# Performance work log

Hardware: AMD Instinct MI355X
Metric: run time of the kernel (lower is better)

The kernel has to match this reference:

```python
import jax, jax.numpy as jnp
import numpy as np
from jax.scipy.linalg import expm

M = 8          # number of mixture models
S = 4          # alphabet size (nucleotides)
N_LEAVES = 20  # taxa
K = 19         # internal nodes (caterpillar binary tree)
BATCH = 200000 # alignment sites


def _build_tree():
    # Caterpillar rooted binary tree: internal node n has children (leaf0, leaf1);
    # internal node n+j has children (internal n+j-1, leaf j+1). T[b, a] = branch length b->a.
    n, k = N_LEAVES, K
    N = n + k
    rng = np.random.default_rng(0)
    T = np.zeros((N, N), dtype=np.float32)
    T[0, n] = rng.uniform(0.05, 1.0)
    T[1, n] = rng.uniform(0.05, 1.0)
    for j in range(1, k):
        a = n + j
        T[a - 1, a] = rng.uniform(0.05, 1.0)
        T[j + 1, a] = rng.uniform(0.05, 1.0)
    return T


def setup_inputs() -> dict:
    key = jax.random.key(0)
    k1, k2 = jax.random.split(key, 2)
    X = jax.random.uniform(k1, (BATCH, N_LEAVES, S), dtype=jnp.float32)
    rates = jax.random.uniform(k2, (M, S * (S - 1) // 2), dtype=jnp.float32)
    pi_inv = jnp.full((M, S - 1), 1.0 / (np.sqrt(S) - 1.0), dtype=jnp.float32)
    rho = jnp.ones((M,), dtype=jnp.float32)
    T = _build_tree()  # numpy: tree structure is static config, not a traced tensor
    return {"X": X, "rates": rates, "pi_inv": pi_inv, "rho": rho, "T": T}


def _inv_stereographic_projection(y):
    ns = jnp.sum(y ** 2, axis=-1)
    return jnp.concatenate([2.0 * y, (ns - 1.0)[..., None]], axis=-1) / (ns + 1.0)[..., None]


def _rate_matrices(rates_sq, pi):
    # rates_sq: [M, s(s-1)/2], pi: [M, s] -> Q: [M, s, s]
    iu, ju = np.triu_indices(S, 1)
    Q = jnp.zeros((M, S, S), rates_sq.dtype).at[:, iu, ju].set(rates_sq)
    Q = Q + jnp.swapaxes(Q, 1, 2)                    # symmetrize
    Q = Q * pi[:, None, :]                           # stationary probabilities
    new_diag = -jnp.sum(Q, axis=2)                   # row sums -> diagonal
    ar = np.arange(S)
    Q = Q.at[:, ar, ar].set(new_diag)
    emut = jnp.maximum(-jnp.sum(pi * new_diag, axis=1), 1e-9)
    return Q / emut[:, None, None]                   # one expected mutation per unit time


def _forward(X, rates, pi_inv, rho, Tnp):
    n, k = N_LEAVES, K
    pi = _inv_stereographic_projection(pi_inv) ** 2          # [M, S]
    Q = _rate_matrices(rates ** 2, pi) * rho[:, None, None]  # [M, S, S]
    es, et = np.nonzero(Tnp)
    A = []  # per internal node: [BATCH, M, S] partial likelihoods
    for a in range(n, n + k):
        ch = es[et == a]
        t = jnp.asarray(Tnp[ch, a])                          # [C] branch lengths
        P = expm(t[:, None, None, None] * Q[None])           # [C, M, S, S] batched small expm
        parts = []
        for i, b in enumerate(ch):
            if b < n:
                parts.append(jnp.einsum('mcd,id->imc', P[i], X[:, b, :]))
            else:
                parts.append(jnp.einsum('mcd,imd->imc', P[i], A[b - n]))
        A.append(jnp.prod(jnp.stack(parts), axis=0))         # Felsenstein pruning product
    return jnp.einsum('imc,mc->im', A[-1], pi)               # [BATCH, M]


def reference(X, rates, pi_inv, rho, T):
    return _forward(X, rates, pi_inv, rho, np.asarray(T))
```

## Files before the change

kernel.cpp:

```cpp
#include <hip/hip_runtime.h>
#include <math.h>

#define MM 8
#define SS 4
#define NLEAF 20
#define KINT 19
#define NBR 38
#define P4 (NBR*MM*4)
#define PFLOATS (P4*4)
#define NNODE 39

typedef float v2f __attribute__((ext_vector_type(2)));
typedef float v4f __attribute__((ext_vector_type(4)));


__device__ __forceinline__ void mat4_mul(const double a[4][4], const double b[4][4], double c[4][4]) {
    #pragma unroll
    for (int i = 0; i < 4; i++)
        #pragma unroll
        for (int j = 0; j < 4; j++) {
            double s = 0.0;
            #pragma unroll
            for (int k = 0; k < 4; k++) s += a[i][k] * b[k][j];
            c[i][j] = s;
        }
}

__global__ void setup_kernel(const float* __restrict__ rates,
                             const float* __restrict__ pi_inv,
                             const float* __restrict__ rho,
                             const float* __restrict__ T,
                             float* __restrict__ ws)
{
    int tid = blockIdx.x * blockDim.x + threadIdx.x;
    if (tid >= NBR * MM) return;
    int m = tid & 7;
    int k = tid >> 3;

    double y0 = pi_inv[m*3+0], y1 = pi_inv[m*3+1], y2 = pi_inv[m*3+2];
    double ns  = y0*y0 + y1*y1 + y2*y2;
    double inv = 1.0 / (ns + 1.0);
    double p[4] = {2.0*y0*inv, 2.0*y1*inv, 2.0*y2*inv, (ns-1.0)*inv};
    #pragma unroll
    for (int i = 0; i < 4; i++) p[i] *= p[i];

    if (k == 0) {
        #pragma unroll
        for (int i = 0; i < 4; i++) ws[PFLOATS + m*4 + i] = (float)p[i];
    }

    double r[6];
    #pragma unroll
    for (int i = 0; i < 6; i++) { double v = rates[m*6+i]; r[i] = v*v; }
    double Q[4][4] = {};
    Q[0][1]=r[0]; Q[0][2]=r[1]; Q[0][3]=r[2]; Q[1][2]=r[3]; Q[1][3]=r[4]; Q[2][3]=r[5];
    #pragma unroll
    for (int i = 0; i < 4; i++)
        #pragma unroll
        for (int j = i+1; j < 4; j++) Q[j][i] = Q[i][j];
    #pragma unroll
    for (int i = 0; i < 4; i++)
        #pragma unroll
        for (int j = 0; j < 4; j++) Q[i][j] *= p[j];
    double emut = 0.0;
    #pragma unroll
    for (int i = 0; i < 4; i++) {
        double rs = 0.0;
        #pragma unroll
        for (int j = 0; j < 4; j++) if (j != i) rs += Q[i][j];
        Q[i][i] = -rs;
        emut += p[i] * rs;
    }
    emut = fmax(emut, 1e-9);
    double scq = (double)rho[m] / emut;

    double t;
    if      (k == 0) t = T[0*NNODE + NLEAF];
    else if (k == 1) t = T[1*NNODE + NLEAF];
    else {
        int j     = k >> 1;
        int node  = NLEAF + j;
        int child = (k & 1) ? (j + 1) : (NLEAF - 1 + j);
        t = T[child*NNODE + node];
    }

    double A[4][4];
    #pragma unroll
    for (int i = 0; i < 4; i++)
        #pragma unroll
        for (int j = 0; j < 4; j++) A[i][j] = Q[i][j] * scq * t;

    double nrm = 0.0;
    #pragma unroll
    for (int i = 0; i < 4; i++) {
        double rs = 0.0;
        #pragma unroll
        for (int j = 0; j < 4; j++) rs += fabs(A[i][j]);
        nrm = fmax(nrm, rs);
    }
    int s = 0;
    if (nrm > 0.0625) s = (int)ceil(log2(nrm * 16.0));
    if (s < 0) s = 0;
    if (s > 60) s = 60;
    double scl = ldexp(1.0, -s);
    double B[4][4];
    #pragma unroll
    for (int i = 0; i < 4; i++)
        #pragma unroll
        for (int j = 0; j < 4; j++) B[i][j] = A[i][j] * scl;

    double E[4][4];
    #pragma unroll
    for (int i = 0; i < 4; i++)
        #pragma unroll
        for (int j = 0; j < 4; j++) E[i][j] = (i == j) ? 1.0 : 0.0;
    for (int kk = 9; kk >= 1; --kk) {
        double Tm[4][4];
        mat4_mul(B, E, Tm);
        double ik = 1.0 / (double)kk;
        #pragma unroll
        for (int i = 0; i < 4; i++)
            #pragma unroll
            for (int j = 0; j < 4; j++) E[i][j] = ((i == j) ? 1.0 : 0.0) + Tm[i][j] * ik;
    }
    for (int q = 0; q < s; q++) {
        double Tm[4][4];
        mat4_mul(E, E, Tm);
        #pragma unroll
        for (int i = 0; i < 4; i++)
            #pragma unroll
            for (int j = 0; j < 4; j++) E[i][j] = Tm[i][j];
    }

    float* Pout = ws + (k*MM + m) * 16;
    #pragma unroll
    for (int d = 0; d < 4; d++)
        #pragma unroll
        for (int c = 0; c < 4; c++) Pout[d*4+c] = (float)E[c][d];
}


#define SHUF(v,a,b) __builtin_shufflevector((v),(v),(a),(b))

__device__ __forceinline__ void matvx(const v4f& c0, const v4f& c1, const v4f& c2, const v4f& c3,
                                      const v4f& x, v2f& lo, v2f& hi)
{
    v2f l = SHUF(c0,0,1) * SHUF(x,0,0);
    v2f h = SHUF(c0,2,3) * SHUF(x,0,0);
    l = __builtin_elementwise_fma(SHUF(c1,0,1), SHUF(x,1,1), l);
    h = __builtin_elementwise_fma(SHUF(c1,2,3), SHUF(x,1,1), h);
    l = __builtin_elementwise_fma(SHUF(c2,0,1), SHUF(x,2,2), l);
    h = __builtin_elementwise_fma(SHUF(c2,2,3), SHUF(x,2,2), h);
    l = __builtin_elementwise_fma(SHUF(c3,0,1), SHUF(x,3,3), l);
    h = __builtin_elementwise_fma(SHUF(c3,2,3), SHUF(x,3,3), h);
    lo = l; hi = h;
}

__device__ __forceinline__ void matvs(const v4f& c0, const v4f& c1, const v4f& c2, const v4f& c3,
                                      v2f alo, v2f ahi, v2f& lo, v2f& hi)
{
    v2f l = SHUF(c0,0,1) * SHUF(alo,0,0);
    v2f h = SHUF(c0,2,3) * SHUF(alo,0,0);
    l = __builtin_elementwise_fma(SHUF(c1,0,1), SHUF(alo,1,1), l);
    h = __builtin_elementwise_fma(SHUF(c1,2,3), SHUF(alo,1,1), h);
    l = __builtin_elementwise_fma(SHUF(c2,0,1), SHUF(ahi,0,0), l);
    h = __builtin_elementwise_fma(SHUF(c2,2,3), SHUF(ahi,0,0), h);
    l = __builtin_elementwise_fma(SHUF(c3,0,1), SHUF(ahi,1,1), l);
    h = __builtin_elementwise_fma(SHUF(c3,2,3), SHUF(ahi,1,1), h);
    lo = l; hi = h;
}

__global__ __launch_bounds__(256) void phylo_kernel(const float* __restrict__ X,
                                                    const float* __restrict__ ws,
                                                    float* __restrict__ out,
                                                    int batch)
{
    const int sraw = blockIdx.x * 256 + threadIdx.x;
    const int site = sraw < batch ? sraw : batch - 1;
    const v4f* __restrict__ P  = (const v4f*)ws;
    const v4f* __restrict__ xs = (const v4f*)X + (size_t)site * 20;

    v2f lo[MM], hi[MM];

    v4f xa = xs[0];
    v4f xb = xs[1];
    #pragma unroll
    for (int m = 0; m < MM; m++) {
        const v4f* __restrict__ P0 = P + (0*MM + m)*4;
        const v4f* __restrict__ P1 = P + (1*MM + m)*4;
        v2f tl, th, ul, uh;
        matvx(P0[0],P0[1],P0[2],P0[3], xa, tl, th);
        matvx(P1[0],P1[1],P1[2],P1[3], xb, ul, uh);
        lo[m] = tl*ul; hi[m] = th*uh;
    }

    xa = xs[2];
    #pragma unroll 1
    for (int j = 1; j < KINT; j++) {
        xb = xa;
        if (j < KINT - 1) xb = xs[j + 2];
        const v4f* __restrict__ PI = P + (2*j*MM)*4;
        const v4f* __restrict__ PL = PI + MM*4;
        #pragma unroll
        for (int m = 0; m < MM; m++) {
            v2f tl, th, ul, uh;
            matvs(PI[m*4+0],PI[m*4+1],PI[m*4+2],PI[m*4+3], lo[m], hi[m], tl, th);
            matvx(PL[m*4+0],PL[m*4+1],PL[m*4+2],PL[m*4+3], xa, ul, uh);
            lo[m] = tl*ul; hi[m] = th*uh;
        }
        xa = xb;
    }

    const v4f* __restrict__ pip = P + P4;
    float r[MM];
    #pragma unroll
    for (int m = 0; m < MM; m++) {
        v4f pim = pip[m];
        v2f s = __builtin_elementwise_fma(hi[m], SHUF(pim,2,3), lo[m] * SHUF(pim,0,1));
        r[m] = s.x + s.y;
    }
    if (sraw < batch) {
        v4f* __restrict__ o4 = (v4f*)(out + (size_t)sraw * MM);
        o4[0] = (v4f){r[0], r[1], r[2], r[3]};
        o4[1] = (v4f){r[4], r[5], r[6], r[7]};
    }
}


extern "C" void kernel_launch(void* const* d_in, const int* in_sizes, int n_in,
                              void* d_out, int out_size, void* d_ws, size_t ws_size,
                              hipStream_t stream)
{
    const float* X      = (const float*)d_in[0];
    const float* rates  = (const float*)d_in[1];
    const float* pi_inv = (const float*)d_in[2];
    const float* rho    = (const float*)d_in[3];
    const float* T      = (const float*)d_in[4];
    float* out = (float*)d_out;
    float* ws  = (float*)d_ws;

    int batch = in_sizes[0] / (NLEAF * SS);

    hipLaunchKernelGGL(setup_kernel, dim3(1), dim3(320), 0, stream,
                       rates, pi_inv, rho, T, ws);

    int grid = (batch + 255) / 256;
    hipLaunchKernelGGL(phylo_kernel, dim3(grid), dim3(256), 0, stream,
                       X, ws, out, batch);
}
```

Measured before the change: 146.9 us.

## Stage transition matrices in LDS and process four sites per thread

```diff
diff --git a/kernel.cpp b/kernel.cpp
--- a/kernel.cpp
+++ b/kernel.cpp
@@ -9,6 +9,9 @@
 #define P4 (NBR*MM*4)
 #define PFLOATS (P4*4)
 #define NNODE 39
+#define SPT 4
+#define BLK 128
+#define SPB (BLK*SPT)
 
 typedef float v2f __attribute__((ext_vector_type(2)));
 typedef float v4f __attribute__((ext_vector_type(4)));
@@ -170,59 +173,88 @@
     lo = l; hi = h;
 }
 
-__global__ __launch_bounds__(256) void phylo_kernel(const float* __restrict__ X,
+__global__ __launch_bounds__(BLK) void phylo_kernel(const float* __restrict__ X,
                                                     const float* __restrict__ ws,
                                                     float* __restrict__ out,
                                                     int batch)
 {
-    const int sraw = blockIdx.x * 256 + threadIdx.x;
-    const int site = sraw < batch ? sraw : batch - 1;
-    const v4f* __restrict__ P  = (const v4f*)ws;
-    const v4f* __restrict__ xs = (const v4f*)X + (size_t)site * 20;
-
-    v2f lo[MM], hi[MM];
-
-    v4f xa = xs[0];
-    v4f xb = xs[1];
+    __shared__ v4f Pl[P4 + MM];
+    const v4f* __restrict__ w4 = (const v4f*)ws;
+    for (int idx = threadIdx.x; idx < P4 + MM; idx += BLK) Pl[idx] = w4[idx];
+    __syncthreads();
+
+    const int t    = threadIdx.x;
+    const int base = blockIdx.x * SPB;
+
+    const v4f* __restrict__ xp[SPT];
+    #pragma unroll
+    for (int k = 0; k < SPT; k++) {
+        int s = base + t + BLK*k;
+        if (s >= batch) s = batch - 1;
+        xp[k] = (const v4f*)X + (size_t)s * 20;
+    }
+
+    v2f lo[SPT][MM], hi[SPT][MM];
+
+    v4f XA[SPT], XB[SPT];
+    #pragma unroll
+    for (int k = 0; k < SPT; k++) { XA[k] = xp[k][0]; XB[k] = xp[k][1]; }
     #pragma unroll
     for (int m = 0; m < MM; m++) {
-        const v4f* __restrict__ P0 = P + (0*MM + m)*4;
-        const v4f* __restrict__ P1 = P + (1*MM + m)*4;
-        v2f tl, th, ul, uh;
-        matvx(P0[0],P0[1],P0[2],P0[3], xa, tl, th);
-        matvx(P1[0],P1[1],P1[2],P1[3], xb, ul, uh);
-        lo[m] = tl*ul; hi[m] = th*uh;
-    }
-
-    xa = xs[2];
+        const v4f* __restrict__ P0 = &Pl[(0*MM + m)*4];
+        const v4f* __restrict__ P1 = &Pl[(1*MM + m)*4];
+        v4f a0=P0[0], a1=P0[1], a2=P0[2], a3=P0[3];
+        v4f e0=P1[0], e1=P1[1], e2=P1[2], e3=P1[3];
+        #pragma unroll
+        for (int k = 0; k < SPT; k++) {
+            v2f tl, th, ul, uh;
+            matvx(a0,a1,a2,a3, XA[k], tl, th);
+            matvx(e0,e1,e2,e3, XB[k], ul, uh);
+            lo[k][m] = tl*ul; hi[k][m] = th*uh;
+        }
+    }
+
+    #pragma unroll
+    for (int k = 0; k < SPT; k++) XA[k] = xp[k][2];
     #pragma unroll 1
     for (int j = 1; j < KINT; j++) {
-        xb = xa;
-        if (j < KINT - 1) xb = xs[j + 2];
-        const v4f* __restrict__ PI = P + (2*j*MM)*4;
+        if (j < KINT - 1) {
+            #pragma unroll
+            for (int k = 0; k < SPT; k++) XB[k] = xp[k][j + 2];
+        }
+        const v4f* __restrict__ PI = &Pl[(2*j*MM)*4];
         const v4f* __restrict__ PL = PI + MM*4;
         #pragma unroll
         for (int m = 0; m < MM; m++) {
-            v2f tl, th, ul, uh;
-            matvs(PI[m*4+0],PI[m*4+1],PI[m*4+2],PI[m*4+3], lo[m], hi[m], tl, th);
-            matvx(PL[m*4+0],PL[m*4+1],PL[m*4+2],PL[m*4+3], xa, ul, uh);
-            lo[m] = tl*ul; hi[m] = th*uh;
-        }
-        xa = xb;
-    }
-
-    const v4f* __restrict__ pip = P + P4;
-    float r[MM];
-    #pragma unroll
-    for (int m = 0; m < MM; m++) {
-        v4f pim = pip[m];
-        v2f s = __builtin_elementwise_fma(hi[m], SHUF(pim,2,3), lo[m] * SHUF(pim,0,1));
-        r[m] = s.x + s.y;
-    }
-    if (sraw < batch) {
-        v4f* __restrict__ o4 = (v4f*)(out + (size_t)sraw * MM);
-        o4[0] = (v4f){r[0], r[1], r[2], r[3]};
-        o4[1] = (v4f){r[4], r[5], r[6], r[7]};
+            v4f ci0=PI[m*4+0], ci1=PI[m*4+1], ci2=PI[m*4+2], ci3=PI[m*4+3];
+            v4f cl0=PL[m*4+0], cl1=PL[m*4+1], cl2=PL[m*4+2], cl3=PL[m*4+3];
+            #pragma unroll
+            for (int k = 0; k < SPT; k++) {
+                v2f tl, th, ul, uh;
+                matvs(ci0,ci1,ci2,ci3, lo[k][m], hi[k][m], tl, th);
+                matvx(cl0,cl1,cl2,cl3, XA[k], ul, uh);
+                lo[k][m] = tl*ul; hi[k][m] = th*uh;
+            }
+        }
+        #pragma unroll
+        for (int k = 0; k < SPT; k++) XA[k] = XB[k];
+    }
+
+    #pragma unroll
+    for (int k = 0; k < SPT; k++) {
+        float r[MM];
+        #pragma unroll
+        for (int m = 0; m < MM; m++) {
+            v4f pim = Pl[P4 + m];
+            v2f s = __builtin_elementwise_fma(hi[k][m], SHUF(pim,2,3), lo[k][m] * SHUF(pim,0,1));
+            r[m] = s.x + s.y;
+        }
+        int st = base + t + BLK*k;
+        if (st < batch) {
+            v4f* __restrict__ o4 = (v4f*)(out + (size_t)st * MM);
+            o4[0] = (v4f){r[0], r[1], r[2], r[3]};
+            o4[1] = (v4f){r[4], r[5], r[6], r[7]};
+        }
     }
 }
 
@@ -244,7 +276,7 @@
     hipLaunchKernelGGL(setup_kernel, dim3(1), dim3(320), 0, stream,
                        rates, pi_inv, rho, T, ws);
 
-    int grid = (batch + 255) / 256;
-    hipLaunchKernelGGL(phylo_kernel, dim3(grid), dim3(256), 0, stream,
+    int grid = (batch + SPB - 1) / SPB;
+    hipLaunchKernelGGL(phylo_kernel, dim3(grid), dim3(BLK), 0, stream,
                        X, ws, out, batch);
 }
```

Result: no change. 148.0 us (+0.7%).

## Process two sites per thread with packed v2f math across sites

Applied to the files above, without the earlier changes.

```diff
diff --git a/kernel.cpp b/kernel.cpp
--- a/kernel.cpp
+++ b/kernel.cpp
@@ -6,9 +6,10 @@
 #define NLEAF 20
 #define KINT 19
 #define NBR 38
-#define P4 (NBR*MM*4)
-#define PFLOATS (P4*4)
+#define PFLOATS (NBR*MM*16)
 #define NNODE 39
+#define BLK 256
+#define SPB 512
 
 typedef float v2f __attribute__((ext_vector_type(2)));
 typedef float v4f __attribute__((ext_vector_type(4)));
@@ -134,95 +135,102 @@
 
     float* Pout = ws + (k*MM + m) * 16;
     #pragma unroll
-    for (int d = 0; d < 4; d++)
-        #pragma unroll
-        for (int c = 0; c < 4; c++) Pout[d*4+c] = (float)E[c][d];
-}
-
-
-#define SHUF(v,a,b) __builtin_shufflevector((v),(v),(a),(b))
-
-__device__ __forceinline__ void matvx(const v4f& c0, const v4f& c1, const v4f& c2, const v4f& c3,
-                                      const v4f& x, v2f& lo, v2f& hi)
-{
-    v2f l = SHUF(c0,0,1) * SHUF(x,0,0);
-    v2f h = SHUF(c0,2,3) * SHUF(x,0,0);
-    l = __builtin_elementwise_fma(SHUF(c1,0,1), SHUF(x,1,1), l);
-    h = __builtin_elementwise_fma(SHUF(c1,2,3), SHUF(x,1,1), h);
-    l = __builtin_elementwise_fma(SHUF(c2,0,1), SHUF(x,2,2), l);
-    h = __builtin_elementwise_fma(SHUF(c2,2,3), SHUF(x,2,2), h);
-    l = __builtin_elementwise_fma(SHUF(c3,0,1), SHUF(x,3,3), l);
-    h = __builtin_elementwise_fma(SHUF(c3,2,3), SHUF(x,3,3), h);
-    lo = l; hi = h;
-}
-
-__device__ __forceinline__ void matvs(const v4f& c0, const v4f& c1, const v4f& c2, const v4f& c3,
-                                      v2f alo, v2f ahi, v2f& lo, v2f& hi)
-{
-    v2f l = SHUF(c0,0,1) * SHUF(alo,0,0);
-    v2f h = SHUF(c0,2,3) * SHUF(alo,0,0);
-    l = __builtin_elementwise_fma(SHUF(c1,0,1), SHUF(alo,1,1), l);
-    h = __builtin_elementwise_fma(SHUF(c1,2,3), SHUF(alo,1,1), h);
-    l = __builtin_elementwise_fma(SHUF(c2,0,1), SHUF(ahi,0,0), l);
-    h = __builtin_elementwise_fma(SHUF(c2,2,3), SHUF(ahi,0,0), h);
-    l = __builtin_elementwise_fma(SHUF(c3,0,1), SHUF(ahi,1,1), l);
-    h = __builtin_elementwise_fma(SHUF(c3,2,3), SHUF(ahi,1,1), h);
-    lo = l; hi = h;
-}
-
-__global__ __launch_bounds__(256) void phylo_kernel(const float* __restrict__ X,
+    for (int c = 0; c < 4; c++)
+        #pragma unroll
+        for (int d = 0; d < 4; d++) Pout[c*4+d] = (float)E[c][d];
+}
+
+
+__device__ __forceinline__ void matvp(const float* __restrict__ Pm,
+                                      const v2f S0, const v2f S1, const v2f S2, const v2f S3,
+                                      v2f t[4])
+{
+    #pragma unroll
+    for (int c = 0; c < 4; c++) {
+        float p0 = Pm[c*4+0], p1 = Pm[c*4+1], p2 = Pm[c*4+2], p3 = Pm[c*4+3];
+        v2f acc = (v2f){p0, p0} * S0;
+        acc = __builtin_elementwise_fma((v2f){p1, p1}, S1, acc);
+        acc = __builtin_elementwise_fma((v2f){p2, p2}, S2, acc);
+        acc = __builtin_elementwise_fma((v2f){p3, p3}, S3, acc);
+        t[c] = acc;
+    }
+}
+
+__global__ __launch_bounds__(BLK) void phylo_kernel(const float* __restrict__ X,
                                                     const float* __restrict__ ws,
                                                     float* __restrict__ out,
                                                     int batch)
 {
-    const int sraw = blockIdx.x * 256 + threadIdx.x;
-    const int site = sraw < batch ? sraw : batch - 1;
-    const v4f* __restrict__ P  = (const v4f*)ws;
-    const v4f* __restrict__ xs = (const v4f*)X + (size_t)site * 20;
-
-    v2f lo[MM], hi[MM];
-
-    v4f xa = xs[0];
-    v4f xb = xs[1];
-    #pragma unroll
-    for (int m = 0; m < MM; m++) {
-        const v4f* __restrict__ P0 = P + (0*MM + m)*4;
-        const v4f* __restrict__ P1 = P + (1*MM + m)*4;
-        v2f tl, th, ul, uh;
-        matvx(P0[0],P0[1],P0[2],P0[3], xa, tl, th);
-        matvx(P1[0],P1[1],P1[2],P1[3], xb, ul, uh);
-        lo[m] = tl*ul; hi[m] = th*uh;
-    }
-
-    xa = xs[2];
+    const int lane = threadIdx.x & 63;
+    const int w    = threadIdx.x >> 6;
+    const int s0   = blockIdx.x * SPB + w * 128 + lane;
+    const int s1   = s0 + 64;
+    const int c0   = s0 < batch ? s0 : batch - 1;
+    const int c1   = s1 < batch ? s1 : batch - 1;
+    const v4f* __restrict__ xs0 = (const v4f*)X + (size_t)c0 * 20;
+    const v4f* __restrict__ xs1 = (const v4f*)X + (size_t)c1 * 20;
+    const float* __restrict__ P = ws;
+
+    v2f S[MM][4];
+
+    {
+        v4f a0 = xs0[0], b0 = xs1[0];
+        v4f a1 = xs0[1], b1 = xs1[1];
+        v2f x0[4], x1[4];
+        #pragma unroll
+        for (int d = 0; d < 4; d++) { x0[d] = (v2f){a0[d], b0[d]}; x1[d] = (v2f){a1[d], b1[d]}; }
+        #pragma unroll
+        for (int m = 0; m < MM; m++) {
+            const float* __restrict__ P0 = P + (0*MM + m)*16;
+            const float* __restrict__ P1 = P + (1*MM + m)*16;
+            v2f t[4], u[4];
+            matvp(P0, x0[0], x0[1], x0[2], x0[3], t);
+            matvp(P1, x1[0], x1[1], x1[2], x1[3], u);
+            #pragma unroll
+            for (int c = 0; c < 4; c++) S[m][c] = t[c] * u[c];
+        }
+    }
+
+    v4f na = xs0[2], nb = xs1[2];
     #pragma unroll 1
     for (int j = 1; j < KINT; j++) {
-        xb = xa;
-        if (j < KINT - 1) xb = xs[j + 2];
-        const v4f* __restrict__ PI = P + (2*j*MM)*4;
-        const v4f* __restrict__ PL = PI + MM*4;
+        v2f xl[4];
+        #pragma unroll
+        for (int d = 0; d < 4; d++) xl[d] = (v2f){na[d], nb[d]};
+        if (j < KINT - 1) { na = xs0[j + 2]; nb = xs1[j + 2]; }
+
+        const float* __restrict__ PI = P + (2*j*MM)*16;
+        const float* __restrict__ PL = PI + MM*16;
         #pragma unroll
         for (int m = 0; m < MM; m++) {
-            v2f tl, th, ul, uh;
-            matvs(PI[m*4+0],PI[m*4+1],PI[m*4+2],PI[m*4+3], lo[m], hi[m], tl, th);
-            matvx(PL[m*4+0],PL[m*4+1],PL[m*4+2],PL[m*4+3], xa, ul, uh);
-            lo[m] = tl*ul; hi[m] = th*uh;
+            v2f t[4], u[4];
+            matvp(PI + m*16, S[m][0], S[m][1], S[m][2], S[m][3], t);
+            matvp(PL + m*16, xl[0], xl[1], xl[2], xl[3], u);
+            #pragma unroll
+            for (int c = 0; c < 4; c++) S[m][c] = t[c] * u[c];
         }
-        xa = xb;
-    }
-
-    const v4f* __restrict__ pip = P + P4;
-    float r[MM];
+    }
+
+    v2f r[MM];
     #pragma unroll
     for (int m = 0; m < MM; m++) {
-        v4f pim = pip[m];
-        v2f s = __builtin_elementwise_fma(hi[m], SHUF(pim,2,3), lo[m] * SHUF(pim,0,1));
-        r[m] = s.x + s.y;
-    }
-    if (sraw < batch) {
-        v4f* __restrict__ o4 = (v4f*)(out + (size_t)sraw * MM);
-        o4[0] = (v4f){r[0], r[1], r[2], r[3]};
-        o4[1] = (v4f){r[4], r[5], r[6], r[7]};
+        const float* __restrict__ pim = P + PFLOATS + m*4;
+        float q0 = pim[0], q1 = pim[1], q2 = pim[2], q3 = pim[3];
+        v2f acc = (v2f){q0, q0} * S[m][0];
+        acc = __builtin_elementwise_fma((v2f){q1, q1}, S[m][1], acc);
+        acc = __builtin_elementwise_fma((v2f){q2, q2}, S[m][2], acc);
+        acc = __builtin_elementwise_fma((v2f){q3, q3}, S[m][3], acc);
+        r[m] = acc;
+    }
+    if (s0 < batch) {
+        v4f* __restrict__ o4 = (v4f*)(out + (size_t)s0 * MM);
+        o4[0] = (v4f){r[0].x, r[1].x, r[2].x, r[3].x};
+        o4[1] = (v4f){r[4].x, r[5].x, r[6].x, r[7].x};
+    }
+    if (s1 < batch) {
+        v4f* __restrict__ o4 = (v4f*)(out + (size_t)s1 * MM);
+        o4[0] = (v4f){r[0].y, r[1].y, r[2].y, r[3].y};
+        o4[1] = (v4f){r[4].y, r[5].y, r[6].y, r[7].y};
     }
 }
 
@@ -244,7 +252,7 @@
     hipLaunchKernelGGL(setup_kernel, dim3(1), dim3(320), 0, stream,
                        rates, pi_inv, rho, T, ws);
 
-    int grid = (batch + 255) / 256;
-    hipLaunchKernelGGL(phylo_kernel, dim3(grid), dim3(256), 0, stream,
+    int grid = (batch + SPB - 1) / SPB;
+    hipLaunchKernelGGL(phylo_kernel, dim3(grid), dim3(BLK), 0, stream,
                        X, ws, out, batch);
 }
```

Measured after the change: 148.7 us. No clear change (+1.3%).

## Split mixture models across waves so each thread handles half the models

Applied to the files above, without the earlier changes.

```diff
diff --git a/kernel.cpp b/kernel.cpp
--- a/kernel.cpp
+++ b/kernel.cpp
@@ -6,9 +6,10 @@
 #define NLEAF 20
 #define KINT 19
 #define NBR 38
-#define P4 (NBR*MM*4)
-#define PFLOATS (P4*4)
+#define PFLOATS (NBR*MM*16)
 #define NNODE 39
+#define BLK 256
+#define SPB 128
 
 typedef float v2f __attribute__((ext_vector_type(2)));
 typedef float v4f __attribute__((ext_vector_type(4)));
@@ -142,87 +143,84 @@
 
 #define SHUF(v,a,b) __builtin_shufflevector((v),(v),(a),(b))
 
-__device__ __forceinline__ void matvx(const v4f& c0, const v4f& c1, const v4f& c2, const v4f& c3,
-                                      const v4f& x, v2f& lo, v2f& hi)
-{
-    v2f l = SHUF(c0,0,1) * SHUF(x,0,0);
-    v2f h = SHUF(c0,2,3) * SHUF(x,0,0);
-    l = __builtin_elementwise_fma(SHUF(c1,0,1), SHUF(x,1,1), l);
-    h = __builtin_elementwise_fma(SHUF(c1,2,3), SHUF(x,1,1), h);
-    l = __builtin_elementwise_fma(SHUF(c2,0,1), SHUF(x,2,2), l);
-    h = __builtin_elementwise_fma(SHUF(c2,2,3), SHUF(x,2,2), h);
-    l = __builtin_elementwise_fma(SHUF(c3,0,1), SHUF(x,3,3), l);
-    h = __builtin_elementwise_fma(SHUF(c3,2,3), SHUF(x,3,3), h);
-    lo = l; hi = h;
-}
-
-__device__ __forceinline__ void matvs(const v4f& c0, const v4f& c1, const v4f& c2, const v4f& c3,
-                                      v2f alo, v2f ahi, v2f& lo, v2f& hi)
-{
-    v2f l = SHUF(c0,0,1) * SHUF(alo,0,0);
-    v2f h = SHUF(c0,2,3) * SHUF(alo,0,0);
-    l = __builtin_elementwise_fma(SHUF(c1,0,1), SHUF(alo,1,1), l);
-    h = __builtin_elementwise_fma(SHUF(c1,2,3), SHUF(alo,1,1), h);
-    l = __builtin_elementwise_fma(SHUF(c2,0,1), SHUF(ahi,0,0), l);
-    h = __builtin_elementwise_fma(SHUF(c2,2,3), SHUF(ahi,0,0), h);
-    l = __builtin_elementwise_fma(SHUF(c3,0,1), SHUF(ahi,1,1), l);
-    h = __builtin_elementwise_fma(SHUF(c3,2,3), SHUF(ahi,1,1), h);
-    lo = l; hi = h;
-}
-
-__global__ __launch_bounds__(256) void phylo_kernel(const float* __restrict__ X,
+__device__ __forceinline__ void matvc(const float* __restrict__ Pm,
+                                      v2f op_lo, v2f op_hi, v2f& tlo, v2f& thi)
+{
+    v2f c0l = (v2f){Pm[0],  Pm[1]},  c0h = (v2f){Pm[2],  Pm[3]};
+    v2f c1l = (v2f){Pm[4],  Pm[5]},  c1h = (v2f){Pm[6],  Pm[7]};
+    v2f c2l = (v2f){Pm[8],  Pm[9]},  c2h = (v2f){Pm[10], Pm[11]};
+    v2f c3l = (v2f){Pm[12], Pm[13]}, c3h = (v2f){Pm[14], Pm[15]};
+    v2f a0 = SHUF(op_lo,0,0), a1 = SHUF(op_lo,1,1);
+    v2f a2 = SHUF(op_hi,0,0), a3 = SHUF(op_hi,1,1);
+    v2f l = c0l * a0, h = c0h * a0;
+    l = __builtin_elementwise_fma(c1l, a1, l); h = __builtin_elementwise_fma(c1h, a1, h);
+    l = __builtin_elementwise_fma(c2l, a2, l); h = __builtin_elementwise_fma(c2h, a2, h);
+    l = __builtin_elementwise_fma(c3l, a3, l); h = __builtin_elementwise_fma(c3h, a3, h);
+    tlo = l; thi = h;
+}
+
+__global__ __launch_bounds__(BLK) void phylo_kernel(const float* __restrict__ X,
                                                     const float* __restrict__ ws,
                                                     float* __restrict__ out,
                                                     int batch)
 {
-    const int sraw = blockIdx.x * 256 + threadIdx.x;
+    const int lane = threadIdx.x & 63;
+    const int w    = threadIdx.x >> 6;
+    const int mh   = __builtin_amdgcn_readfirstlane(w >> 1);
+    const int sg   = w & 1;
+    const int sraw = blockIdx.x * SPB + sg * 64 + lane;
     const int site = sraw < batch ? sraw : batch - 1;
-    const v4f* __restrict__ P  = (const v4f*)ws;
     const v4f* __restrict__ xs = (const v4f*)X + (size_t)site * 20;
-
-    v2f lo[MM], hi[MM];
-
-    v4f xa = xs[0];
-    v4f xb = xs[1];
-    #pragma unroll
-    for (int m = 0; m < MM; m++) {
-        const v4f* __restrict__ P0 = P + (0*MM + m)*4;
-        const v4f* __restrict__ P1 = P + (1*MM + m)*4;
-        v2f tl, th, ul, uh;
-        matvx(P0[0],P0[1],P0[2],P0[3], xa, tl, th);
-        matvx(P1[0],P1[1],P1[2],P1[3], xb, ul, uh);
-        lo[m] = tl*ul; hi[m] = th*uh;
-    }
-
-    xa = xs[2];
+    const float* __restrict__ P = ws;
+    const int mbase = mh * 4;
+
+    v2f Slo[4], Shi[4];
+
+    {
+        v4f x0 = xs[0], x1 = xs[1];
+        v2f x0l = (v2f){x0.x, x0.y}, x0h = (v2f){x0.z, x0.w};
+        v2f x1l = (v2f){x1.x, x1.y}, x1h = (v2f){x1.z, x1.w};
+        #pragma unroll
+        for (int mi = 0; mi < 4; mi++) {
+            const float* __restrict__ P0 = P + (0*MM + mbase + mi)*16;
+            const float* __restrict__ P1 = P + (1*MM + mbase + mi)*16;
+            v2f tl, th, ul, uh;
+            matvc(P0, x0l, x0h, tl, th);
+            matvc(P1, x1l, x1h, ul, uh);
+            Slo[mi] = tl*ul; Shi[mi] = th*uh;
+        }
+    }
+
+    v4f xa = xs[2];
     #pragma unroll 1
     for (int j = 1; j < KINT; j++) {
-        xb = xa;
-        if (j < KINT - 1) xb = xs[j + 2];
-        const v4f* __restrict__ PI = P + (2*j*MM)*4;
-        const v4f* __restrict__ PL = PI + MM*4;
-        #pragma unroll
-        for (int m = 0; m < MM; m++) {
+        v4f xn = xa;
+        if (j < KINT - 1) xn = xs[j + 2];
+        v2f xl = (v2f){xa.x, xa.y}, xh = (v2f){xa.z, xa.w};
+        const float* __restrict__ PI = P + (2*j*MM + mbase)*16;
+        const float* __restrict__ PL = PI + MM*16;
+        #pragma unroll
+        for (int mi = 0; mi < 4; mi++) {
             v2f tl, th, ul, uh;
-            matvs(PI[m*4+0],PI[m*4+1],PI[m*4+2],PI[m*4+3], lo[m], hi[m], tl, th);
-            matvx(PL[m*4+0],PL[m*4+1],PL[m*4+2],PL[m*4+3], xa, ul, uh);
-            lo[m] = tl*ul; hi[m] = th*uh;
+            matvc(PI + mi*16, Slo[mi], Shi[mi], tl, th);
+            matvc(PL + mi*16, xl, xh, ul, uh);
+            Slo[mi] = tl*ul; Shi[mi] = th*uh;
         }
-        xa = xb;
-    }
-
-    const v4f* __restrict__ pip = P + P4;
-    float r[MM];
-    #pragma unroll
-    for (int m = 0; m < MM; m++) {
-        v4f pim = pip[m];
-        v2f s = __builtin_elementwise_fma(hi[m], SHUF(pim,2,3), lo[m] * SHUF(pim,0,1));
-        r[m] = s.x + s.y;
+        xa = xn;
+    }
+
+    const float* __restrict__ pip = P + PFLOATS + mbase*4;
+    float r[4];
+    #pragma unroll
+    for (int mi = 0; mi < 4; mi++) {
+        v2f plo = (v2f){pip[mi*4+0], pip[mi*4+1]};
+        v2f phi = (v2f){pip[mi*4+2], pip[mi*4+3]};
+        v2f s = __builtin_elementwise_fma(Shi[mi], phi, Slo[mi] * plo);
+        r[mi] = s.x + s.y;
     }
     if (sraw < batch) {
-        v4f* __restrict__ o4 = (v4f*)(out + (size_t)sraw * MM);
+        v4f* __restrict__ o4 = (v4f*)(out + (size_t)sraw * MM + mbase);
         o4[0] = (v4f){r[0], r[1], r[2], r[3]};
-        o4[1] = (v4f){r[4], r[5], r[6], r[7]};
     }
 }
 
@@ -244,7 +242,7 @@
     hipLaunchKernelGGL(setup_kernel, dim3(1), dim3(320), 0, stream,
                        rates, pi_inv, rho, T, ws);
 
-    int grid = (batch + 255) / 256;
-    hipLaunchKernelGGL(phylo_kernel, dim3(grid), dim3(256), 0, stream,
+    int grid = (batch + SPB - 1) / SPB;
+    hipLaunchKernelGGL(phylo_kernel, dim3(grid), dim3(BLK), 0, stream,
                        X, ws, out, batch);
 }
```

Result: faster. 135.6 us (-7.7%).
